# Performance work log

Hardware: AMD Instinct MI355X
Metric: run time of the kernel (lower is better)

Reference implementation:

```python
import jax, jax.numpy as jnp
import numpy as np

B, T, D_MODEL, N_HEADS = 4, 2048, 1024, 16
HEAD_DIM = D_MODEL // N_HEADS  # 64
ROPE_BASE = 10000.0


def setup_inputs() -> dict:
    key = jax.random.key(0)
    k1, k2, k3 = jax.random.split(key, 3)
    x = jax.random.normal(k1, (B, T, D_MODEL), dtype=jnp.float32)
    # nn.Linear(d, 3d, bias=False) and nn.Linear(d, d, bias=False), stored as (in, out)
    w_qkv = jax.random.normal(k2, (D_MODEL, 3 * D_MODEL), dtype=jnp.float32) / np.sqrt(D_MODEL)
    w_proj = jax.random.normal(k3, (D_MODEL, D_MODEL), dtype=jnp.float32) / np.sqrt(D_MODEL)
    # standard RoPE tables: (T, HEAD_DIM/2)
    inv_freq = 1.0 / (ROPE_BASE ** (np.arange(0, HEAD_DIM, 2, dtype=np.float32) / HEAD_DIM))
    ang = np.arange(T, dtype=np.float32)[:, None] * inv_freq[None, :]
    cos = jnp.asarray(np.cos(ang), dtype=jnp.float32)
    sin = jnp.asarray(np.sin(ang), dtype=jnp.float32)
    return {"x": x, "cos": cos, "sin": sin, "w_qkv": w_qkv, "w_proj": w_proj}


def _apply_rope(x, cos, sin):
    # x: (B, H, T, D); cos/sin: (T, D/2) broadcast over (B, H)
    x1 = x[..., 0::2]
    x2 = x[..., 1::2]
    r1 = x1 * cos - x2 * sin
    r2 = x2 * cos + x1 * sin
    # interleave back: out[..., 0::2]=r1, out[..., 1::2]=r2
    return jnp.stack([r1, r2], axis=-1).reshape(x.shape)


def reference(x, cos, sin, w_qkv, w_proj):
    b, t, _ = x.shape
    qkv = (x @ w_qkv).reshape(b, t, 3, N_HEADS, HEAD_DIM).transpose(2, 0, 3, 1, 4)
    q, k, v = qkv[0], qkv[1], qkv[2]  # each (B, H, T, D)
    q = _apply_rope(q, cos[:t], sin[:t])
    k = _apply_rope(k, cos[:t], sin[:t])
    scale = 1.0 / jnp.sqrt(jnp.asarray(HEAD_DIM, dtype=x.dtype))
    scores = jnp.einsum("bhqd,bhkd->bhqk", q, k) * scale
    causal = jnp.tril(jnp.ones((t, t), dtype=bool))
    scores = jnp.where(causal, scores, jnp.finfo(scores.dtype).min)
    attn = jax.nn.softmax(scores, axis=-1)
    out = jnp.einsum("bhqk,bhkd->bhqd", attn, v)
    out = out.transpose(0, 2, 1, 3).reshape(b, t, D_MODEL)
    return out @ w_proj
```

## Files before the change

kernel.cpp:

```cpp
#include <hip/hip_runtime.h>
#include <cstdint>
#include <cstddef>

typedef __attribute__((ext_vector_type(8))) short bf16x8;
typedef __attribute__((ext_vector_type(4))) float f32x4;
typedef __attribute__((ext_vector_type(16))) float f32x16;
typedef __attribute__((ext_vector_type(4))) unsigned int u32x4;

#define B_ 4
#define T_ 2048
#define DM 1024
#define NH 16
#define HD 64

static __device__ __forceinline__ unsigned short f2bf(float f) {
  union { float f; unsigned int u; } v; v.f = f;
  unsigned int r = v.u + 0x7FFFu + ((v.u >> 16) & 1u);
  return (unsigned short)(r >> 16);
}
static __device__ __forceinline__ float exp2_fast(float x) {
  float r;
  asm volatile("v_exp_f32 %0, %1" : "=v"(r) : "v"(x));
  return r;
}
static __device__ __forceinline__ unsigned int cvt_pk_bf16(float a, float b) {
  unsigned int r;
  asm("v_cvt_pk_bf16_f32 %0, %1, %2" : "=v"(r) : "v"(a), "v"(b));
  return r;
}

static __device__ __forceinline__ void gll16(const void* g, void* l) {
  __builtin_amdgcn_global_load_lds(
      (const __attribute__((address_space(1))) void*)g,
      (__attribute__((address_space(3))) void*)l, 16, 0, 0);
}

#define BARRIER() do { asm volatile("" ::: "memory"); __builtin_amdgcn_s_barrier(); asm volatile("" ::: "memory"); } while (0)

__global__ __launch_bounds__(256) void prep_kernel(
    const float* __restrict__ x, unsigned short* __restrict__ x16,
    const float* __restrict__ w_qkv, unsigned short* __restrict__ wqkvT,
    const float* __restrict__ w_proj, unsigned short* __restrict__ wprojT) {
  __shared__ unsigned short tile[32][33];
  const int bid = blockIdx.x;
  const int tid = threadIdx.x;
  if (bid < 2048) {
    const int n8 = (B_ * T_ * DM) / 8;
    for (int i = bid * 256 + tid; i < n8; i += 2048 * 256) {
      const float4* p = (const float4*)(x + (size_t)i * 8);
      float4 a = p[0], b = p[1];
      u32x4 o;
      o[0] = cvt_pk_bf16(a.x, a.y);
      o[1] = cvt_pk_bf16(a.z, a.w);
      o[2] = cvt_pk_bf16(b.x, b.y);
      o[3] = cvt_pk_bf16(b.z, b.w);
      *(u32x4*)(x16 + (size_t)i * 8) = o;
    }
    return;
  }
  const float* in;
  unsigned short* out;
  int R, C, bx, by;
  if (bid < 5120) {
    const int b2 = bid - 2048;
    in = w_qkv; out = wqkvT; R = 1024; C = 3072;
    bx = b2 % 96; by = b2 / 96;
  } else {
    const int b2 = bid - 5120;
    in = w_proj; out = wprojT; R = 1024; C = 1024;
    bx = b2 % 32; by = b2 / 32;
  }
  const int c0 = bx * 32, r0 = by * 32;
  const int tx = tid & 31, ty = tid >> 5;
#pragma unroll
  for (int j = 0; j < 32; j += 8) {
    float v = in[(size_t)(r0 + ty + j) * C + c0 + tx];
    tile[tx][ty + j] = f2bf(v);
  }
  __syncthreads();
#pragma unroll
  for (int j = 0; j < 32; j += 8) {
    out[(size_t)(c0 + ty + j) * R + r0 + tx] = tile[ty + j][tx];
  }
}

#define GEMM_MAIN2(As, Bs, Agl, Bgl, acc)                                    \
  {                                                                          \
    const char* gA = (const char*)(Agl) +                                    \
                     (size_t)(m0 + (tid >> 3)) * 2048 +                      \
                     (((tid & 7) ^ ((tid >> 3) & 7)) << 4);                  \
    const char* gB = (const char*)(Bgl) +                                    \
                     (size_t)(n0 + (tid >> 3)) * 2048 +                      \
                     (((tid & 7) ^ ((tid >> 3) & 7)) << 4);                  \
    _Pragma("unroll") for (int i = 0; i < 4; i++) {                          \
      gll16(gA + (size_t)i * 65536, (char*)(As) + i * 4096 + w * 1024);      \
      gll16(gB + (size_t)i * 65536, (char*)(Bs) + i * 4096 + w * 1024);      \
    }                                                                        \
    for (int t = 0; t < 16; t++) {                                           \
      const int cur = (t & 1) << 14;                                         \
      if (t < 15) {                                                          \
        const int nxt = ((t + 1) & 1) << 14;                                 \
        const int k0 = (t + 1) * 128;                                        \
        _Pragma("unroll") for (int i = 0; i < 4; i++) {                      \
          gll16(gA + (size_t)i * 65536 + k0,                                 \
                (char*)(As) + nxt + i * 4096 + w * 1024);                    \
          gll16(gB + (size_t)i * 65536 + k0,                                 \
                (char*)(Bs) + nxt + i * 4096 + w * 1024);                    \
        }                                                                    \
        asm volatile("s_waitcnt vmcnt(8)" ::: "memory");                     \
      } else {                                                               \
        asm volatile("s_waitcnt vmcnt(0)" ::: "memory");                     \
      }                                                                      \
      BARRIER();                                                             \
      _Pragma("unroll") for (int kk = 0; kk < 2; kk++) {                     \
        bf16x8 af[4], bfr[4];                                                \
        const int ko = (kk * 64 + lg * 16) ^ ((lr & 7) << 4);                \
        _Pragma("unroll") for (int mi = 0; mi < 4; mi++)                     \
            af[mi] = *(const bf16x8*)((const char*)(As) + cur +              \
                                      (wr * 64 + mi * 16 + lr) * 128 + ko);  \
        _Pragma("unroll") for (int ni = 0; ni < 4; ni++)                     \
            bfr[ni] = *(const bf16x8*)((const char*)(Bs) + cur +             \
                                       (wc * 64 + ni * 16 + lr) * 128 + ko); \
        _Pragma("unroll") for (int mi = 0; mi < 4; mi++)                     \
            _Pragma("unroll") for (int ni = 0; ni < 4; ni++)                 \
                acc[mi][ni] = __builtin_amdgcn_mfma_f32_16x16x32_bf16(       \
                    af[mi], bfr[ni], acc[mi][ni], 0, 0, 0);                  \
      }                                                                      \
      BARRIER();                                                             \
    }                                                                        \
  }

__global__ __launch_bounds__(256, 2) void gemm_qkv(
    const unsigned short* __restrict__ A, const unsigned short* __restrict__ Bt,
    const float* __restrict__ cosT, const float* __restrict__ sinT,
    unsigned short* __restrict__ Qo, unsigned short* __restrict__ Ko,
    unsigned short* __restrict__ VTo) {
  __shared__ __align__(16) unsigned short As[2 * 8192];
  __shared__ __align__(16) unsigned short Bs[2 * 8192];
  const int bid = blockIdx.x;
  const int xcd = bid & 7;
  const int cc = bid >> 3;
  const int m0 = (xcd * 8 + (cc & 7)) * 128;
  const int n0 = (cc >> 3) * 128;
  const int tid = threadIdx.x;
  const int w = tid >> 6, l = tid & 63;
  const int wr = w >> 1, wc = w & 1;
  const int lr = l & 15, lg = l >> 4;
  f32x4 acc[4][4];
#pragma unroll
  for (int i = 0; i < 4; i++)
#pragma unroll
    for (int j = 0; j < 4; j++) acc[i][j] = (f32x4)0.f;

  GEMM_MAIN2(As, Bs, A, Bt, acc)

  {
    float4* cosL4 = (float4*)As;
    float4* sinL4 = (float4*)Bs;
    const float4* cg = (const float4*)(cosT + (size_t)(m0 & 2047) * 32);
    const float4* sg = (const float4*)(sinT + (size_t)(m0 & 2047) * 32);
#pragma unroll
    for (int i = 0; i < 4; i++) {
      const int c = tid + i * 256;
      const int rw = c >> 3, f4 = c & 7;
      const int slot = rw * 8 + (f4 ^ (((rw >> 2) & 3) << 1));
      cosL4[slot] = cg[c];
      sinL4[slot] = sg[c];
    }
  }
  BARRIER();
  const float* cosL = (const float*)As;
  const float* sinL = (const float*)Bs;

#pragma unroll
  for (int mi = 0; mi < 4; mi++) {
#pragma unroll
    for (int ni = 0; ni < 4; ni++) {
      const int col = n0 + wc * 64 + ni * 16 + lr;
      const int which = col >> 10;
      const int hd = col & 1023;
      const int h = hd >> 6, d = hd & 63;
      const int fi = d >> 1;
      const float sgn = (lr & 1) ? 1.0f : -1.0f;
      const float qsc = (which == 0) ? 0.18033688f : 1.0f;
      float vv[4];
#pragma unroll
      for (int r = 0; r < 4; r++) {
        const int row = m0 + wr * 64 + mi * 16 + lg * 4 + r;
        float v = acc[mi][ni][r];
        if (which < 2) {
          float p = __shfl_xor(v, 1, 64);
          const int fj = fi ^ (((row >> 2) & 3) << 3);
          const int lo = (row & 127) * 32 + fj;
          v = (v * cosL[lo] + sgn * p * sinL[lo]) * qsc;
        }
        vv[r] = v;
      }
      const unsigned int pk0 = cvt_pk_bf16(vv[0], vv[1]);
      const unsigned int pk1 = cvt_pk_bf16(vv[2], vv[3]);
#pragma unroll
      for (int r = 0; r < 4; r++) {
        const int row = m0 + wr * 64 + mi * 16 + lg * 4 + r;
        const int b = row >> 11, tt = row & 2047;
        const unsigned int pk = (r < 2) ? pk0 : pk1;
        const unsigned short bv =
            (unsigned short)((r & 1) ? (pk >> 16) : (pk & 0xFFFFu));
        size_t bh = (size_t)(b * NH + h);
        if (which == 0)
          Qo[(bh * T_ + tt) * HD + d] = bv;
        else if (which == 1)
          Ko[(bh * T_ + tt) * HD + d] = bv;
        else
          VTo[(bh * HD + d) * T_ + tt] = bv;
      }
    }
  }
}

__global__ __launch_bounds__(256, 2) void gemm_proj(
    const unsigned short* __restrict__ A, const unsigned short* __restrict__ Bt,
    float* __restrict__ C) {
  __shared__ __align__(16) unsigned short As[2 * 8192];
  __shared__ __align__(16) unsigned short Bs[2 * 8192];
  const int bid = blockIdx.x;
  const int xcd = bid & 7;
  const int cc = bid >> 3;
  const int m0 = (xcd * 8 + cc / 8) * 128;
  const int n0 = (cc % 8) * 128;
  const int tid = threadIdx.x;
  const int w = tid >> 6, l = tid & 63;
  const int wr = w >> 1, wc = w & 1;
  const int lr = l & 15, lg = l >> 4;
  f32x4 acc[4][4];
#pragma unroll
  for (int i = 0; i < 4; i++)
#pragma unroll
    for (int j = 0; j < 4; j++) acc[i][j] = (f32x4)0.f;

  GEMM_MAIN2(As, Bs, A, Bt, acc)

#pragma unroll
  for (int mi = 0; mi < 4; mi++) {
#pragma unroll
    for (int ni = 0; ni < 4; ni++) {
      const int col = n0 + wc * 64 + ni * 16 + lr;
#pragma unroll
      for (int r = 0; r < 4; r++) {
        const int row = m0 + wr * 64 + mi * 16 + lg * 4 + r;
        C[(size_t)row * 1024 + col] = acc[mi][ni][r];
      }
    }
  }
}

__global__ __launch_bounds__(256, 3) void attn_kernel(
    const unsigned short* __restrict__ Q, const unsigned short* __restrict__ K,
    const unsigned short* __restrict__ VT, unsigned short* __restrict__ O) {
  __shared__ __align__(16) unsigned short Ks[3][4096];
  __shared__ __align__(16) unsigned short Vs[3][4096];

  const int blk = blockIdx.x;
  const int bh = (blk & 7) * 8 + ((blk >> 3) & 7);
  const int r4 = blk >> 8, g4 = (blk >> 6) & 3;
  const int qt = (r4 == 0) ? (15 - g4)
               : (r4 == 1) ? (8 + g4)
               : (r4 == 2) ? (7 - g4)
                           : g4;
  const int b = bh >> 4, h = bh & 15;
  const int tid = threadIdx.x;
  const int w = tid >> 6, l = tid & 63;
  const int q31 = l & 31, h5 = l >> 5;
  const int q0w = qt * 128 + w * 32;
  const int q_abs = q0w + q31;

  const unsigned short* Qb = Q + (size_t)bh * T_ * HD;
  const char* Kc = (const char*)(K + (size_t)bh * T_ * HD);
  const char* Vc = (const char*)(VT + (size_t)bh * HD * T_);

  const int c0 = (w * 2) * 64 + l;
  const int c1 = (w * 2 + 1) * 64 + l;
  const int r0 = c0 >> 3, r1 = c1 >> 3;
  const int sw0 = ((c0 & 7) * 16) ^ ((r0 & 7) << 4);
  const int sw1 = ((c1 & 7) * 16) ^ ((r1 & 7) << 4);
  const char* pK0 = Kc + r0 * 128 + sw0;
  const char* pK1 = Kc + r1 * 128 + sw1;
  const char* pV0 = Vc + (size_t)r0 * (T_ * 2) + sw0;
  const char* pV1 = Vc + (size_t)r1 * (T_ * 2) + sw1;

#define SK(buf, tile)                                                       \
  do {                                                                      \
    size_t kb = (size_t)(tile) * 8192;                                      \
    gll16(pK0 + kb, (char*)Ks[buf] + (w * 2) * 1024);                       \
    gll16(pK1 + kb, (char*)Ks[buf] + (w * 2 + 1) * 1024);                   \
  } while (0)
#define SV(buf, tile)                                                       \
  do {                                                                      \
    size_t vb = (size_t)(tile) * 128;                                       \
    gll16(pV0 + vb, (char*)Vs[buf] + (w * 2) * 1024);                       \
    gll16(pV1 + vb, (char*)Vs[buf] + (w * 2 + 1) * 1024);                   \
  } while (0)

  bf16x8 qf[4];
#pragma unroll
  for (int ks4 = 0; ks4 < 4; ks4++)
    qf[ks4] = *(const bf16x8*)(Qb + (size_t)q_abs * HD + ks4 * 16 + h5 * 8);

  f32x16 ot0 = (f32x16)0.f, ot1 = (f32x16)0.f;
  float m_reg = -1e30f, lrow = 0.f;

  const int nt = 2 * qt + 2;
  const int jmax = q0w >> 6;

  SK(0, 0);
  SV(0, 0);
  if (nt > 1) {
    SK(1, 1);
    SV(1, 1);
  }
  if (nt > 2) {
    SK(2, 2);
    SV(2, 2);
  }

  int cur3 = 0;
  for (int j = 0; j < nt; j++) {
    if (j <= nt - 3) {
      asm volatile("s_waitcnt vmcnt(8)" ::: "memory");
    } else if (j == nt - 2) {
      asm volatile("s_waitcnt vmcnt(4)" ::: "memory");
    } else {
      asm volatile("s_waitcnt vmcnt(0)" ::: "memory");
    }
    BARRIER();
    if (j <= jmax) {
      f32x16 st[2];
      st[0] = (f32x16)0.f;
      st[1] = (f32x16)0.f;
      __builtin_amdgcn_s_setprio(1);
#pragma unroll
      for (int sub = 0; sub < 2; sub++) {
        const int row = sub * 32 + q31;
        const int sw = (row & 7) << 4;
#pragma unroll
        for (int ks4 = 0; ks4 < 4; ks4++) {
          bf16x8 kf = *(const bf16x8*)((const char*)Ks[cur3] + row * 128 +
                                       ((ks4 * 32 + h5 * 16) ^ sw));
          st[sub] = __builtin_amdgcn_mfma_f32_32x32x16_bf16(kf, qf[ks4],
                                                            st[sub], 0, 0, 0);
        }
      }
      __builtin_amdgcn_s_setprio(0);
      if (j == jmax) {
        const int t0 = j * 64;
#pragma unroll
        for (int sub = 0; sub < 2; sub++)
#pragma unroll
          for (int r = 0; r < 16; r++) {
            int kv_abs = t0 + sub * 32 + (r & 3) + 8 * (r >> 2) + 4 * h5;
            if (kv_abs > q_abs) st[sub][r] = -1e30f;
          }
      }
      float pmax;
      {
        float q0m = -1e30f, q1m = -1e30f;
#pragma unroll
        for (int r = 0; r < 16; r += 4) {
          q0m = fmaxf(q0m, fmaxf(fmaxf(st[0][r], st[0][r + 1]),
                                 fmaxf(st[0][r + 2], st[0][r + 3])));
          q1m = fmaxf(q1m, fmaxf(fmaxf(st[1][r], st[1][r + 1]),
                                 fmaxf(st[1][r + 2], st[1][r + 3])));
        }
        pmax = fmaxf(q0m, q1m);
      }
      pmax = fmaxf(pmax, __shfl_xor(pmax, 32, 64));
      const int defer = __all(pmax - m_reg <= 8.0f);
      if (!defer) {
        float mnew = fmaxf(m_reg, pmax);
        float alpha = exp2_fast(m_reg - mnew);
        m_reg = mnew;
        lrow *= alpha;
#pragma unroll
        for (int r = 0; r < 16; r++) {
          ot0[r] *= alpha;
          ot1[r] *= alpha;
        }
      }
      float rsum = 0.f;
#pragma unroll
      for (int sub = 0; sub < 2; sub++)
#pragma unroll
        for (int r = 0; r < 16; r++) {
          float p = exp2_fast(st[sub][r] - m_reg);
          st[sub][r] = p;
          rsum += p;
        }
      rsum += __shfl_xor(rsum, 32, 64);
      lrow += rsum;
      unsigned int pk[2][8];
#pragma unroll
      for (int sub = 0; sub < 2; sub++)
#pragma unroll
        for (int g = 0; g < 4; g++) {
          pk[sub][2 * g] = cvt_pk_bf16(st[sub][4 * g + 0], st[sub][4 * g + 1]);
          pk[sub][2 * g + 1] =
              cvt_pk_bf16(st[sub][4 * g + 2], st[sub][4 * g + 3]);
        }
      bf16x8 pf[4];
#pragma unroll
      for (int sub = 0; sub < 2; sub++)
#pragma unroll
        for (int s = 0; s < 2; s++) {
          unsigned int a0 = pk[sub][4 * s + 0], a1 = pk[sub][4 * s + 1];
          unsigned int b0 = pk[sub][4 * s + 2], b1 = pk[sub][4 * s + 3];
          unsigned int send0 = h5 ? a0 : b0, send1 = h5 ? a1 : b1;
          unsigned int sh0 = (unsigned int)__shfl_xor((int)send0, 32, 64);
          unsigned int sh1 = (unsigned int)__shfl_xor((int)send1, 32, 64);
          unsigned int ow0 = h5 ? b0 : a0, ow1 = h5 ? b1 : a1;
          u32x4 fu;
          fu[0] = h5 ? sh0 : ow0;
          fu[1] = h5 ? sh1 : ow1;
          fu[2] = h5 ? ow0 : sh0;
          fu[3] = h5 ? ow1 : sh1;
          pf[sub * 2 + s] = *(bf16x8*)&fu;
        }
      __builtin_amdgcn_s_setprio(1);
#pragma unroll
      for (int ks = 0; ks < 4; ks++) {
        const int colb = ks * 32 + h5 * 16;
        {
          const int row = q31;
          bf16x8 vf = *(const bf16x8*)((const char*)Vs[cur3] + row * 128 +
                                       (colb ^ ((row & 7) << 4)));
          ot0 = __builtin_amdgcn_mfma_f32_32x32x16_bf16(vf, pf[ks], ot0, 0, 0, 0);
        }
        {
          const int row = 32 + q31;
          bf16x8 vf = *(const bf16x8*)((const char*)Vs[cur3] + row * 128 +
                                       (colb ^ ((row & 7) << 4)));
          ot1 = __builtin_amdgcn_mfma_f32_32x32x16_bf16(vf, pf[ks], ot1, 0, 0, 0);
        }
      }
      __builtin_amdgcn_s_setprio(0);
    }
    BARRIER();
    if (j + 3 < nt) {
      SK(cur3, j + 3);
      SV(cur3, j + 3);
    }
    cur3 = (cur3 == 2) ? 0 : cur3 + 1;
  }

  const float rcpl = 1.0f / lrow;
  unsigned short* Orow = O + ((size_t)b * T_ + q_abs) * DM + h * HD;
#pragma unroll
  for (int rg = 0; rg < 4; rg++) {
    uint2 s0;
    s0.x = cvt_pk_bf16(ot0[4 * rg + 0] * rcpl, ot0[4 * rg + 1] * rcpl);
    s0.y = cvt_pk_bf16(ot0[4 * rg + 2] * rcpl, ot0[4 * rg + 3] * rcpl);
    *(uint2*)(Orow + 8 * rg + 4 * h5) = s0;
    uint2 s1;
    s1.x = cvt_pk_bf16(ot1[4 * rg + 0] * rcpl, ot1[4 * rg + 1] * rcpl);
    s1.y = cvt_pk_bf16(ot1[4 * rg + 2] * rcpl, ot1[4 * rg + 3] * rcpl);
    *(uint2*)(Orow + 32 + 8 * rg + 4 * h5) = s1;
  }
#undef SK
#undef SV
}

extern "C" void kernel_launch(void* const* d_in, const int* in_sizes, int n_in,
                              void* d_out, int out_size, void* d_ws,
                              size_t ws_size, hipStream_t stream) {
  const float* x = (const float*)d_in[0];
  const float* cosT = (const float*)d_in[1];
  const float* sinT = (const float*)d_in[2];
  const float* w_qkv = (const float*)d_in[3];
  const float* w_proj = (const float*)d_in[4];
  float* out = (float*)d_out;

  char* ws = (char*)d_ws;
  unsigned short* x16 = (unsigned short*)(ws);
  unsigned short* wqkvT = (unsigned short*)(ws + (16 << 20));
  unsigned short* wprojT = (unsigned short*)(ws + (22 << 20));
  unsigned short* Qb = (unsigned short*)(ws + (24 << 20));
  unsigned short* Kb = (unsigned short*)(ws + (40 << 20));
  unsigned short* VTb = (unsigned short*)(ws + (56 << 20));
  unsigned short* Ob = x16;

  prep_kernel<<<6144, 256, 0, stream>>>(x, x16, w_qkv, wqkvT, w_proj, wprojT);
  gemm_qkv<<<1536, 256, 0, stream>>>(x16, wqkvT, cosT, sinT, Qb, Kb, VTb);
  attn_kernel<<<1024, 256, 0, stream>>>(Qb, Kb, VTb, Ob);
  gemm_proj<<<512, 256, 0, stream>>>(Ob, wprojT, out);
}
```

Baseline: 178.7 us.

## Use single-buffered GEMM main loop in QKV kernel to raise occupancy

Switches the QKV projection GEMM from a double-buffered LDS pipeline to a single-buffered loop that waits for each tile's loads before computing. This halves the LDS footprint (32KB vs 64KB) and raises the launch-bounds occupancy target from 2 to 3 blocks per CU, aiming to hide latency through more resident waves rather than software prefetch. It gives up overlap of global loads with MFMA compute within a block.

```diff
diff --git a/kernel.cpp b/kernel.cpp
--- a/kernel.cpp
+++ b/kernel.cpp
@@ -36,6 +36,7 @@
 }
 
 #define BARRIER() do { asm volatile("" ::: "memory"); __builtin_amdgcn_s_barrier(); asm volatile("" ::: "memory"); } while (0)
+#define WAITV0() asm volatile("s_waitcnt vmcnt(0)" ::: "memory")
 
 __global__ __launch_bounds__(256) void prep_kernel(
     const float* __restrict__ x, unsigned short* __restrict__ x16,
@@ -83,6 +84,39 @@
     out[(size_t)(c0 + ty + j) * R + r0 + tx] = tile[ty + j][tx];
   }
 }
+
+#define GEMM_MAIN(As, Bs, Agl, Bgl, acc)                                     \
+  {                                                                          \
+    const char* gA = (const char*)(Agl) +                                    \
+                     (size_t)(m0 + (tid >> 3)) * 2048 +                      \
+                     (((tid & 7) ^ ((tid >> 3) & 7)) << 4);                  \
+    const char* gB = (const char*)(Bgl) +                                    \
+                     (size_t)(n0 + (tid >> 3)) * 2048 +                      \
+                     (((tid & 7) ^ ((tid >> 3) & 7)) << 4);                  \
+    for (int k0 = 0; k0 < 2048; k0 += 128) {                                 \
+      _Pragma("unroll") for (int i = 0; i < 4; i++) {                        \
+        gll16(gA + (size_t)i * 65536 + k0, (char*)(As) + i * 4096 + w * 1024);\
+        gll16(gB + (size_t)i * 65536 + k0, (char*)(Bs) + i * 4096 + w * 1024);\
+      }                                                                      \
+      WAITV0();                                                              \
+      BARRIER();                                                             \
+      _Pragma("unroll") for (int kk = 0; kk < 2; kk++) {                     \
+        bf16x8 af[4], bfr[4];                                                \
+        const int ko = (kk * 64 + lg * 16) ^ ((lr & 7) << 4);                \
+        _Pragma("unroll") for (int mi = 0; mi < 4; mi++)                     \
+            af[mi] = *(const bf16x8*)((const char*)(As) +                    \
+                                      (wr * 64 + mi * 16 + lr) * 128 + ko);  \
+        _Pragma("unroll") for (int ni = 0; ni < 4; ni++)                     \
+            bfr[ni] = *(const bf16x8*)((const char*)(Bs) +                   \
+                                       (wc * 64 + ni * 16 + lr) * 128 + ko); \
+        _Pragma("unroll") for (int mi = 0; mi < 4; mi++)                     \
+            _Pragma("unroll") for (int ni = 0; ni < 4; ni++)                 \
+                acc[mi][ni] = __builtin_amdgcn_mfma_f32_16x16x32_bf16(       \
+                    af[mi], bfr[ni], acc[mi][ni], 0, 0, 0);                  \
+      }                                                                      \
+      BARRIER();                                                             \
+    }                                                                        \
+  }
 
 #define GEMM_MAIN2(As, Bs, Agl, Bgl, acc)                                    \
   {                                                                          \
@@ -130,13 +164,13 @@
     }                                                                        \
   }
 
-__global__ __launch_bounds__(256, 2) void gemm_qkv(
+__global__ __launch_bounds__(256, 3) void gemm_qkv(
     const unsigned short* __restrict__ A, const unsigned short* __restrict__ Bt,
     const float* __restrict__ cosT, const float* __restrict__ sinT,
     unsigned short* __restrict__ Qo, unsigned short* __restrict__ Ko,
     unsigned short* __restrict__ VTo) {
-  __shared__ __align__(16) unsigned short As[2 * 8192];
-  __shared__ __align__(16) unsigned short Bs[2 * 8192];
+  __shared__ __align__(16) unsigned short As[128 * 64];
+  __shared__ __align__(16) unsigned short Bs[128 * 64];
   const int bid = blockIdx.x;
   const int xcd = bid & 7;
   const int cc = bid >> 3;
@@ -152,7 +186,7 @@
 #pragma unroll
     for (int j = 0; j < 4; j++) acc[i][j] = (f32x4)0.f;
 
-  GEMM_MAIN2(As, Bs, A, Bt, acc)
+  GEMM_MAIN(As, Bs, A, Bt, acc)
 
   {
     float4* cosL4 = (float4*)As;
```

After: 172.9 us. 1.03x faster.

## Rewrite QKV GEMM as 256x256 tile with 8-wave quadrant-pipelined K loop

Applied to the files above, without the earlier changes.

The QKV projection GEMM moves from 128x128 tiles with 4 waves to 256x256 tiles with 8 waves and a 128KB LDS double buffer. Each K step is split into four quadrant phases that interleave global-to-LDS loads for the next step with MFMA work on the current one, using explicit vmcnt waits and s_setprio around MFMA bursts. The larger tile is meant to raise operand reuse and cut global and LDS traffic per FLOP. In exchange, the grid drops to 384 blocks of 512 threads, which gives low occupancy and an uneven tail wave across the CUs. The RoPE epilogue is adapted to the bigger tile.

```diff
diff --git a/kernel.cpp b/kernel.cpp
--- a/kernel.cpp
+++ b/kernel.cpp
@@ -36,6 +36,7 @@
 }
 
 #define BARRIER() do { asm volatile("" ::: "memory"); __builtin_amdgcn_s_barrier(); asm volatile("" ::: "memory"); } while (0)
+#define WAITV0() asm volatile("s_waitcnt vmcnt(0)" ::: "memory")
 
 __global__ __launch_bounds__(256) void prep_kernel(
     const float* __restrict__ x, unsigned short* __restrict__ x16,
@@ -130,38 +131,172 @@
     }                                                                        \
   }
 
-__global__ __launch_bounds__(256, 2) void gemm_qkv(
+__global__ __launch_bounds__(512, 2) void gemm_qkv(
     const unsigned short* __restrict__ A, const unsigned short* __restrict__ Bt,
     const float* __restrict__ cosT, const float* __restrict__ sinT,
     unsigned short* __restrict__ Qo, unsigned short* __restrict__ Ko,
     unsigned short* __restrict__ VTo) {
-  __shared__ __align__(16) unsigned short As[2 * 8192];
-  __shared__ __align__(16) unsigned short Bs[2 * 8192];
+  __shared__ __align__(16) char lds[131072];
   const int bid = blockIdx.x;
   const int xcd = bid & 7;
   const int cc = bid >> 3;
-  const int m0 = (xcd * 8 + (cc & 7)) * 128;
-  const int n0 = (cc >> 3) * 128;
+  const int m0 = (xcd * 4 + (cc & 3)) * 256;
+  const int n0 = (cc >> 2) * 256;
   const int tid = threadIdx.x;
   const int w = tid >> 6, l = tid & 63;
-  const int wr = w >> 1, wc = w & 1;
+  const int wr = w >> 2, wc = w & 3;
   const int lr = l & 15, lg = l >> 4;
-  f32x4 acc[4][4];
-#pragma unroll
-  for (int i = 0; i < 4; i++)
+
+  const char* gsrc[4][2];
+  int ldso[4][2];
+  {
+    const int cb = tid & 7;
+#pragma unroll
+    for (int i = 0; i < 2; i++) {
+      const int rp = (tid + i * 512) >> 3;
+      const int rAe = rp + (rp & 64);
+      const int rBn0 = ((rp >> 5) << 6) + (rp & 31);
+      const int rAo = rp + 64 + (rp & 64);
+      const int rBn1 = rBn0 + 32;
+      gsrc[0][i] = (const char*)A + (size_t)(m0 + rAe) * 2048 + ((cb ^ (rAe & 7)) << 4);
+      gsrc[1][i] = (const char*)Bt + (size_t)(n0 + rBn0) * 2048 + ((cb ^ (rBn0 & 7)) << 4);
+      gsrc[2][i] = (const char*)A + (size_t)(m0 + rAo) * 2048 + ((cb ^ (rAo & 7)) << 4);
+      gsrc[3][i] = (const char*)Bt + (size_t)(n0 + rBn1) * 2048 + ((cb ^ (rBn1 & 7)) << 4);
+      const int rp0 = w * 8 + i * 64;
+      const int fAe = rp0 + (rp0 & 64);
+      const int fBn0 = ((rp0 >> 5) << 6) + (rp0 & 31);
+      const int fAo = rp0 + 64 + (rp0 & 64);
+      const int fBn1 = fBn0 + 32;
+      ldso[0][i] = fAe * 128;
+      ldso[1][i] = 65536 + fBn0 * 128;
+      ldso[2][i] = fAo * 128;
+      ldso[3][i] = 65536 + fBn1 * 128;
+    }
+  }
+
+#define STG(q, i, kb, nb) gll16(gsrc[q][i] + (kb), lds + ldso[q][i] + (nb) * 32768)
+
+  f32x4 acc[8][4];
+#pragma unroll
+  for (int i = 0; i < 8; i++)
 #pragma unroll
     for (int j = 0; j < 4; j++) acc[i][j] = (f32x4)0.f;
 
-  GEMM_MAIN2(As, Bs, A, Bt, acc)
+#pragma unroll
+  for (int q = 0; q < 4; q++) {
+    STG(q, 0, 0, 0);
+    STG(q, 1, 0, 0);
+  }
+  WAITV0();
+  BARRIER();
+
+  const int aswz = (lr & 7) << 4;
+  for (int t = 0; t < 16; t++) {
+    const int cur = t & 1, nb = cur ^ 1;
+    const int kb1 = (t + 1) * 128;
+    const char* Ab = lds + cur * 32768;
+    const char* Bb = lds + 65536 + cur * 32768;
+    bf16x8 af[4][2], bfr[2][2];
+
+    if (t < 15) { STG(0, 0, kb1, nb); STG(0, 1, kb1, nb); }
+    if (t < 15) asm volatile("s_waitcnt vmcnt(6)" ::: "memory");
+    else        asm volatile("s_waitcnt vmcnt(4)" ::: "memory");
+    BARRIER();
+#pragma unroll
+    for (int i = 0; i < 4; i++)
+#pragma unroll
+      for (int kk = 0; kk < 2; kk++)
+        af[i][kk] = *(const bf16x8*)(Ab + (wr * 128 + i * 16 + lr) * 128 +
+                                     ((kk * 64 + lg * 16) ^ aswz));
+#pragma unroll
+    for (int j = 0; j < 2; j++)
+#pragma unroll
+      for (int kk = 0; kk < 2; kk++)
+        bfr[j][kk] = *(const bf16x8*)(Bb + (wc * 64 + j * 16 + lr) * 128 +
+                                      ((kk * 64 + lg * 16) ^ aswz));
+    __builtin_amdgcn_s_setprio(1);
+#pragma unroll
+    for (int kk = 0; kk < 2; kk++)
+#pragma unroll
+      for (int i = 0; i < 4; i++)
+#pragma unroll
+        for (int j = 0; j < 2; j++)
+          acc[i][j] = __builtin_amdgcn_mfma_f32_16x16x32_bf16(
+              af[i][kk], bfr[j][kk], acc[i][j], 0, 0, 0);
+    __builtin_amdgcn_s_setprio(0);
+
+    if (t < 15) { STG(1, 0, kb1, nb); STG(1, 1, kb1, nb); }
+    if (t < 15) asm volatile("s_waitcnt vmcnt(6)" ::: "memory");
+    else        asm volatile("s_waitcnt vmcnt(2)" ::: "memory");
+    BARRIER();
+#pragma unroll
+    for (int i = 0; i < 4; i++)
+#pragma unroll
+      for (int kk = 0; kk < 2; kk++)
+        af[i][kk] = *(const bf16x8*)(Ab + (wr * 128 + 64 + i * 16 + lr) * 128 +
+                                     ((kk * 64 + lg * 16) ^ aswz));
+    __builtin_amdgcn_s_setprio(1);
+#pragma unroll
+    for (int kk = 0; kk < 2; kk++)
+#pragma unroll
+      for (int i = 0; i < 4; i++)
+#pragma unroll
+        for (int j = 0; j < 2; j++)
+          acc[4 + i][j] = __builtin_amdgcn_mfma_f32_16x16x32_bf16(
+              af[i][kk], bfr[j][kk], acc[4 + i][j], 0, 0, 0);
+    __builtin_amdgcn_s_setprio(0);
+
+    if (t < 15) { STG(2, 0, kb1, nb); STG(2, 1, kb1, nb); }
+    if (t < 15) asm volatile("s_waitcnt vmcnt(6)" ::: "memory");
+    else        asm volatile("s_waitcnt vmcnt(0)" ::: "memory");
+    BARRIER();
+#pragma unroll
+    for (int j = 0; j < 2; j++)
+#pragma unroll
+      for (int kk = 0; kk < 2; kk++)
+        bfr[j][kk] = *(const bf16x8*)(Bb + (wc * 64 + 32 + j * 16 + lr) * 128 +
+                                      ((kk * 64 + lg * 16) ^ aswz));
+    __builtin_amdgcn_s_setprio(1);
+#pragma unroll
+    for (int kk = 0; kk < 2; kk++)
+#pragma unroll
+      for (int i = 0; i < 4; i++)
+#pragma unroll
+        for (int j = 0; j < 2; j++)
+          acc[4 + i][2 + j] = __builtin_amdgcn_mfma_f32_16x16x32_bf16(
+              af[i][kk], bfr[j][kk], acc[4 + i][2 + j], 0, 0, 0);
+    __builtin_amdgcn_s_setprio(0);
+
+    if (t < 15) { STG(3, 0, kb1, nb); STG(3, 1, kb1, nb); }
+    BARRIER();
+#pragma unroll
+    for (int i = 0; i < 4; i++)
+#pragma unroll
+      for (int kk = 0; kk < 2; kk++)
+        af[i][kk] = *(const bf16x8*)(Ab + (wr * 128 + i * 16 + lr) * 128 +
+                                     ((kk * 64 + lg * 16) ^ aswz));
+    __builtin_amdgcn_s_setprio(1);
+#pragma unroll
+    for (int kk = 0; kk < 2; kk++)
+#pragma unroll
+      for (int i = 0; i < 4; i++)
+#pragma unroll
+        for (int j = 0; j < 2; j++)
+          acc[i][2 + j] = __builtin_amdgcn_mfma_f32_16x16x32_bf16(
+              af[i][kk], bfr[j][kk], acc[i][2 + j], 0, 0, 0);
+    __builtin_amdgcn_s_setprio(0);
+    BARRIER();
+  }
+#undef STG
 
   {
-    float4* cosL4 = (float4*)As;
-    float4* sinL4 = (float4*)Bs;
+    float4* cosL4 = (float4*)lds;
+    float4* sinL4 = (float4*)(lds + 65536);
     const float4* cg = (const float4*)(cosT + (size_t)(m0 & 2047) * 32);
     const float4* sg = (const float4*)(sinT + (size_t)(m0 & 2047) * 32);
 #pragma unroll
     for (int i = 0; i < 4; i++) {
-      const int c = tid + i * 256;
+      const int c = tid + i * 512;
       const int rw = c >> 3, f4 = c & 7;
       const int slot = rw * 8 + (f4 ^ (((rw >> 2) & 3) << 1));
       cosL4[slot] = cg[c];
@@ -169,11 +304,11 @@
     }
   }
   BARRIER();
-  const float* cosL = (const float*)As;
-  const float* sinL = (const float*)Bs;
-
-#pragma unroll
-  for (int mi = 0; mi < 4; mi++) {
+  const float* cosL = (const float*)lds;
+  const float* sinL = (const float*)(lds + 65536);
+
+#pragma unroll
+  for (int mi = 0; mi < 8; mi++) {
 #pragma unroll
     for (int ni = 0; ni < 4; ni++) {
       const int col = n0 + wc * 64 + ni * 16 + lr;
@@ -186,12 +321,12 @@
       float vv[4];
 #pragma unroll
       for (int r = 0; r < 4; r++) {
-        const int row = m0 + wr * 64 + mi * 16 + lg * 4 + r;
+        const int row = m0 + wr * 128 + mi * 16 + lg * 4 + r;
         float v = acc[mi][ni][r];
         if (which < 2) {
           float p = __shfl_xor(v, 1, 64);
           const int fj = fi ^ (((row >> 2) & 3) << 3);
-          const int lo = (row & 127) * 32 + fj;
+          const int lo = (row & 255) * 32 + fj;
           v = (v * cosL[lo] + sgn * p * sinL[lo]) * qsc;
         }
         vv[r] = v;
@@ -200,7 +335,7 @@
       const unsigned int pk1 = cvt_pk_bf16(vv[2], vv[3]);
 #pragma unroll
       for (int r = 0; r < 4; r++) {
-        const int row = m0 + wr * 64 + mi * 16 + lg * 4 + r;
+        const int row = m0 + wr * 128 + mi * 16 + lg * 4 + r;
         const int b = row >> 11, tt = row & 2047;
         const unsigned int pk = (r < 2) ? pk0 : pk1;
         const unsigned short bv =
@@ -487,7 +622,7 @@
   unsigned short* Ob = x16;
 
   prep_kernel<<<6144, 256, 0, stream>>>(x, x16, w_qkv, wqkvT, w_proj, wprojT);
-  gemm_qkv<<<1536, 256, 0, stream>>>(x16, wqkvT, cosT, sinT, Qb, Kb, VTb);
+  gemm_qkv<<<384, 512, 0, stream>>>(x16, wqkvT, cosT, sinT, Qb, Kb, VTb);
   attn_kernel<<<1024, 256, 0, stream>>>(Qb, Kb, VTb, Ob);
   gemm_proj<<<512, 256, 0, stream>>>(Ob, wprojT, out);
 }
```

Result: slower. 192.4 us (+7.7%).
